# Kernel tuning notes

Hardware: AMD Instinct MI355X
Metric: run time of the kernel (lower is better)

Reference implementation:

```python
import jax, jax.numpy as jnp
import numpy as np

B, S, H = 4, 2048, 2048
NH, NKV, HD = 16, 4, 128  # heads, kv heads, head_dim; group g = NH // NKV = 4
ROPE_BASE = 10000.0


def rotate_half(x):
    x1, x2 = jnp.split(x, 2, axis=-1)
    return jnp.concatenate([-x2, x1], axis=-1)


def setup_inputs() -> dict:
    key = jax.random.key(0)
    k1, k2, k3 = jax.random.split(key, 3)
    hidden_states = jax.random.normal(k1, (B, S, H), dtype=jnp.float32)
    # additive causal mask [B, 1, S, S]: 0 on/below diagonal, large negative above
    causal = jnp.tril(jnp.ones((S, S), dtype=bool))
    attention_mask = jnp.where(causal, 0.0, -1e9).astype(jnp.float32)
    attention_mask = jnp.broadcast_to(attention_mask[None, None], (B, 1, S, S))
    # RoPE tables [S, HD]
    inv_freq = 1.0 / (ROPE_BASE ** (np.arange(0, HD, 2, dtype=np.float32) / HD))
    pos = np.arange(S, dtype=np.float32)
    freqs = np.outer(pos, inv_freq)                       # [S, HD/2]
    emb = np.concatenate([freqs, freqs], axis=-1)         # [S, HD]
    rope_cos = jnp.asarray(np.cos(emb), dtype=jnp.float32)
    rope_sin = jnp.asarray(np.sin(emb), dtype=jnp.float32)
    w_attn = jax.random.normal(k2, (H, H + 2 * NKV * HD), dtype=jnp.float32) * 0.02
    w_proj = jax.random.normal(k3, (H, H), dtype=jnp.float32) * 0.02
    return {"hidden_states": hidden_states, "attention_mask": attention_mask,
            "rope_cos": rope_cos, "rope_sin": rope_sin,
            "w_attn": w_attn, "w_proj": w_proj}


def reference(hidden_states, attention_mask, rope_cos, rope_sin, w_attn, w_proj):
    g = NH // NKV
    qkv = jnp.einsum('bsh,hf->bsf', hidden_states, w_attn)          # [B,S,(g+2)*NKV*HD]
    qkv = qkv.reshape(B, S, NKV, (g + 2) * HD)
    q, k, v = jnp.split(qkv, [g * HD, (g + 1) * HD], axis=-1)
    q = q.reshape(B, S, NH, HD).transpose(0, 2, 1, 3)               # [B,NH,S,HD]
    k = k.transpose(0, 2, 1, 3)                                     # [B,NKV,S,HD]
    v = v.transpose(0, 2, 1, 3)                                     # [B,NKV,S,HD]
    cos = rope_cos[None, None]                                      # [1,1,S,HD]
    sin = rope_sin[None, None]
    q = q * cos + rotate_half(q) * sin
    k = k * cos + rotate_half(k) * sin
    # repeat kv heads to match query heads (repeat_interleave semantics)
    k = jnp.repeat(k, g, axis=1)                                    # [B,NH,S,HD]
    v = jnp.repeat(v, g, axis=1)
    scale = 1.0 / (HD ** 0.5)
    scores = jnp.einsum('bhqd,bhkd->bhqk', q, k) * scale + attention_mask
    attn = jax.nn.softmax(scores.astype(jnp.float32), axis=-1).astype(q.dtype)
    out = jnp.einsum('bhqk,bhkd->bhqd', attn, v)                    # [B,NH,S,HD]
    out = out.transpose(0, 2, 1, 3).reshape(B, S, NH * HD)
    return jnp.einsum('bsh,hf->bsf', out, w_proj)
```

## Files before the change

kernel.cpp:

```cpp
#include <hip/hip_runtime.h>
#include <hip/hip_bf16.h>
#include <stdint.h>

#define B_   4
#define S_   2048
#define H_   2048
#define NH_  16
#define NKV_ 4
#define HD_  128
#define F_   3072

typedef __bf16 bf16x8 __attribute__((ext_vector_type(8)));
typedef float  f32x4  __attribute__((ext_vector_type(4)));
typedef unsigned short u16;

#define GLOAD_LDS16(gp, lp)                                                             \
  __builtin_amdgcn_global_load_lds((const __attribute__((address_space(1))) void*)(gp), \
                                   (__attribute__((address_space(3))) void*)(lp), 16, 0, 0)

__device__ __forceinline__ u16 f2bf(float f) {
  union { float f; uint32_t u; } v; v.f = f;
  uint32_t r = (v.u + 0x7FFFu + ((v.u >> 16) & 1u)) >> 16;
  return (u16)r;
}
__device__ __forceinline__ float bf2f(u16 u) {
  union { uint32_t u; float f; } v; v.u = ((uint32_t)u) << 16;
  return v.f;
}

__global__ void k_cvt_bf16(const float* __restrict__ in, u16* __restrict__ out, int n4) {
  int i = blockIdx.x * 256 + threadIdx.x;
  if (i >= n4) return;
  float4 v = ((const float4*)in)[i];
  union { u16 s[4]; uint2 u; } o;
  o.s[0] = f2bf(v.x); o.s[1] = f2bf(v.y); o.s[2] = f2bf(v.z); o.s[3] = f2bf(v.w);
  ((uint2*)out)[i] = o.u;
}

__global__ void k_transpose_cvt(const float* __restrict__ in, u16* __restrict__ out, int R, int C) {
  __shared__ u16 tile[64][68];
  int c0 = blockIdx.x * 64, r0 = blockIdx.y * 64;
  int t = threadIdx.x;
#pragma unroll
  for (int j = 0; j < 16; ++j) {
    int e = j * 256 + t;
    int r = e >> 6, c = e & 63;
    tile[r][c] = f2bf(in[(size_t)(r0 + r) * C + (c0 + c)]);
  }
  __syncthreads();
#pragma unroll
  for (int j = 0; j < 16; ++j) {
    int e = j * 256 + t;
    int c = e >> 6, r = e & 63;
    out[(size_t)(c0 + c) * R + (r0 + r)] = tile[r][c];
  }
}

template <bool OUTF32>
__global__ __launch_bounds__(256) void k_gemm_bt(const u16* __restrict__ A, const u16* __restrict__ BT,
                                                 void* __restrict__ Cv, int M, int N, int K) {
  __shared__ u16 lA[128 * 64];
  __shared__ u16 lB[128 * 64];
  int t = threadIdx.x, w = t >> 6, l = t & 63, c = l & 15, g = l >> 4;
  int bn = blockIdx.x * 128, bm = blockIdx.y * 128;
  int wm = (w >> 1) * 64, wn = (w & 1) * 64;

  f32x4 acc[4][4];
#pragma unroll
  for (int mi = 0; mi < 4; ++mi)
#pragma unroll
    for (int ni = 0; ni < 4; ++ni) acc[mi][ni] = (f32x4){0.f, 0.f, 0.f, 0.f};

  int nk = K >> 6;
  int srow = l >> 3, scol = (l & 7) * 8;
  for (int kt = 0; kt < nk; ++kt) {
    int k0 = kt << 6;
    __syncthreads();
#pragma unroll
    for (int i = 0; i < 4; ++i) {
      int ch = i * 4 + w;
      int row = ch * 8 + srow;
      GLOAD_LDS16(&A [(size_t)(bm + row) * K + k0 + scol], &lA[ch * 512]);
      GLOAD_LDS16(&BT[(size_t)(bn + row) * K + k0 + scol], &lB[ch * 512]);
    }
    asm volatile("s_waitcnt vmcnt(0)" ::: "memory");
    __syncthreads();
#pragma unroll
    for (int s = 0; s < 2; ++s) {
      bf16x8 af[4], bfr[4];
#pragma unroll
      for (int mi = 0; mi < 4; ++mi)
        af[mi] = *(const bf16x8*)&lA[(wm + mi * 16 + c) * 64 + (s * 4 + g) * 8];
#pragma unroll
      for (int ni = 0; ni < 4; ++ni)
        bfr[ni] = *(const bf16x8*)&lB[(wn + ni * 16 + c) * 64 + (s * 4 + g) * 8];
#pragma unroll
      for (int mi = 0; mi < 4; ++mi)
#pragma unroll
        for (int ni = 0; ni < 4; ++ni)
          acc[mi][ni] = __builtin_amdgcn_mfma_f32_16x16x32_bf16(af[mi], bfr[ni], acc[mi][ni], 0, 0, 0);
    }
  }
#pragma unroll
  for (int mi = 0; mi < 4; ++mi)
#pragma unroll
    for (int ni = 0; ni < 4; ++ni)
#pragma unroll
      for (int r = 0; r < 4; ++r) {
        size_t row = (size_t)bm + wm + mi * 16 + 4 * g + r;
        size_t col = (size_t)bn + wn + ni * 16 + c;
        if constexpr (OUTF32) ((float*)Cv)[row * N + col] = acc[mi][ni][r];
        else                  ((u16*)Cv)  [row * N + col] = f2bf(acc[mi][ni][r]);
      }
}

__global__ void k_rope_qk(const u16* __restrict__ qkv, const float* __restrict__ ct,
                          const float* __restrict__ st, u16* __restrict__ Q, u16* __restrict__ Kd) {
  size_t idx = (size_t)blockIdx.x * 256 + threadIdx.x;
  const size_t NQ = (size_t)B_ * NH_ * S_ * HD_;
  int d, s, row, col; size_t oidx; u16* dst;
  if (idx < NQ) {
    d = (int)(idx & 127); s = (int)((idx >> 7) & (S_ - 1));
    int h = (int)((idx >> 18) & 15); int b = (int)(idx >> 22);
    row = b * S_ + s;
    col = (h >> 2) * 768 + (h & 3) * 128 + d;
    dst = Q; oidx = idx;
  } else {
    size_t i2 = idx - NQ;
    d = (int)(i2 & 127); s = (int)((i2 >> 7) & (S_ - 1));
    int kvh = (int)((i2 >> 18) & 3); int b = (int)(i2 >> 20);
    row = b * S_ + s;
    col = kvh * 768 + 512 + d;
    dst = Kd; oidx = i2;
  }
  float x  = bf2f(qkv[(size_t)row * F_ + col]);
  float xr = (d < 64) ? -bf2f(qkv[(size_t)row * F_ + col + 64])
                      :  bf2f(qkv[(size_t)row * F_ + col - 64]);
  float o = x * ct[s * HD_ + d] + xr * st[s * HD_ + d];
  dst[oidx] = f2bf(o);
}

__global__ void k_transpose_v(const u16* __restrict__ qkv, u16* __restrict__ Vt) {
  __shared__ u16 tile[64][136];
  int s0 = blockIdx.x * 64;
  int b = blockIdx.y >> 2, kvh = blockIdx.y & 3;
  int t = threadIdx.x;
  const u16* src = qkv + (size_t)(b * S_ + s0) * F_ + kvh * 768 + 640;
#pragma unroll
  for (int j = 0; j < 4; ++j) {
    int e = j * 256 + t;
    int sl = e >> 4, ch = e & 15;
    *(uint4*)&tile[sl][ch * 8] = *(const uint4*)&src[(size_t)sl * F_ + ch * 8];
  }
  __syncthreads();
  u16* dstb = Vt + (size_t)(b * NKV_ + kvh) * HD_ * S_;
#pragma unroll
  for (int j = 0; j < 4; ++j) {
    int e = j * 256 + t;
    int d = e & 127, sc = e >> 7;
    u16 tmp[8];
#pragma unroll
    for (int i = 0; i < 8; ++i) tmp[i] = tile[sc * 8 + i][d];
    *(uint4*)&dstb[(size_t)d * S_ + s0 + sc * 8] = *(const uint4*)tmp;
  }
}

__global__ __launch_bounds__(256, 4) void k_flash(const u16* __restrict__ Q, const u16* __restrict__ K,
                                                  const u16* __restrict__ Vt, u16* __restrict__ O) {
  __shared__ u16 lK[64 * 128];
  __shared__ u16 lV[128 * 64];
  __shared__ u16 lP[4][16 * 64];
  int t = threadIdx.x, w = t >> 6, l = t & 63, c = l & 15, g = l >> 4;
  int qb = (int)(gridDim.x - 1 - blockIdx.x);
  int bh = blockIdx.y;
  int b = bh >> 4, h = bh & 15, kvh = h >> 2;
  int qw = qb * 64 + w * 16;
  const u16* Qb = Q  + (size_t)(b * NH_  + h)   * S_ * HD_;
  const u16* Kb = K  + (size_t)(b * NKV_ + kvh) * S_ * HD_;
  const u16* Vb = Vt + (size_t)(b * NKV_ + kvh) * HD_ * S_;

  bf16x8 qf[4];
#pragma unroll
  for (int sl = 0; sl < 4; ++sl)
    qf[sl] = *(const bf16x8*)&Qb[(size_t)(qw + c) * HD_ + sl * 32 + g * 8];

  f32x4 oacc[8];
#pragma unroll
  for (int nd = 0; nd < 8; ++nd) oacc[nd] = (f32x4){0.f, 0.f, 0.f, 0.f};
  float m_run = -1e30f, l_run = 0.f;

  int ntiles = qb + 1;
  int krl = l >> 4;
  int vrl = l >> 3;

  for (int kt = 0; kt < ntiles; ++kt) {
    int kv0 = kt * 64;
    __syncthreads();
#pragma unroll
    for (int i = 0; i < 4; ++i) {
      int ch = i * 4 + w;
      int rrK = ch * 4 + krl;
      int jK  = (l & 15) ^ (rrK & 15);
      GLOAD_LDS16(&Kb[(size_t)(kv0 + rrK) * HD_ + jK * 8], &lK[ch * 512]);
      int rdV = ch * 8 + vrl;
      int jV  = (l & 7) ^ (rdV & 7);
      GLOAD_LDS16(&Vb[(size_t)rdV * S_ + kv0 + jV * 8], &lV[ch * 512]);
    }
    asm volatile("s_waitcnt vmcnt(0)" ::: "memory");
    __syncthreads();
    if (kv0 <= qw + 15) {
      f32x4 sc[4];
#pragma unroll
      for (int f = 0; f < 4; ++f) sc[f] = (f32x4){0.f, 0.f, 0.f, 0.f};
#pragma unroll
      for (int sl = 0; sl < 4; ++sl)
#pragma unroll
        for (int f = 0; f < 4; ++f) {
          bf16x8 kf = *(const bf16x8*)&lK[(f * 16 + c) * 128 + (((sl * 4 + g) ^ c) * 8)];
          sc[f] = __builtin_amdgcn_mfma_f32_16x16x32_bf16(kf, qf[sl], sc[f], 0, 0, 0);
        }
      const float SCL = 0.088388347648318447f * 1.4426950408889634f;
      bool partial = (kv0 + 63 > qw);
      float pvv[4][4];
      float pm = -1e30f;
#pragma unroll
      for (int f = 0; f < 4; ++f)
#pragma unroll
        for (int r = 0; r < 4; ++r) {
          float v = sc[f][r] * SCL;
          if (partial && (kv0 + f * 16 + 4 * g + r > qw + c)) v = -1e30f;
          pvv[f][r] = v;
          pm = fmaxf(pm, v);
        }
      pm = fmaxf(pm, __shfl_xor(pm, 16));
      pm = fmaxf(pm, __shfl_xor(pm, 32));
      float m_new = fmaxf(m_run, pm);
      float alpha = exp2f(m_run - m_new);
      float ps = 0.f;
#pragma unroll
      for (int f = 0; f < 4; ++f)
#pragma unroll
        for (int r = 0; r < 4; ++r) {
          float p = exp2f(pvv[f][r] - m_new);
          pvv[f][r] = p;
          ps += p;
        }
      ps += __shfl_xor(ps, 16);
      ps += __shfl_xor(ps, 32);
      l_run = l_run * alpha + ps;
      m_run = m_new;
#pragma unroll
      for (int r = 0; r < 4; ++r) {
        float ar = __shfl(alpha, 4 * g + r);
#pragma unroll
        for (int nd = 0; nd < 8; ++nd) oacc[nd][r] *= ar;
      }
      char* Pw = (char*)&lP[w][0];
#pragma unroll
      for (int f = 0; f < 4; ++f) {
        int base = f * 32 + g * 8;
        int chunk = base >> 4, within = base & 15;
        uint32_t p01 = (uint32_t)f2bf(pvv[f][0]) | ((uint32_t)f2bf(pvv[f][1]) << 16);
        uint32_t p23 = (uint32_t)f2bf(pvv[f][2]) | ((uint32_t)f2bf(pvv[f][3]) << 16);
        int rowb = c * 128 + ((chunk ^ (c & 7)) << 4) + within;
        *(uint32_t*)(Pw + rowb)     = p01;
        *(uint32_t*)(Pw + rowb + 4) = p23;
      }
#pragma unroll
      for (int ks = 0; ks < 2; ++ks) {
        bf16x8 pf = *(const bf16x8*)(Pw + c * 128 + (((ks * 4 + g) ^ (c & 7)) << 4));
#pragma unroll
        for (int nd = 0; nd < 8; ++nd) {
          int rowv = nd * 16 + c;
          bf16x8 vf = *(const bf16x8*)&lV[rowv * 64 + (((ks * 4 + g) ^ (c & 7)) * 8)];
          oacc[nd] = __builtin_amdgcn_mfma_f32_16x16x32_bf16(pf, vf, oacc[nd], 0, 0, 0);
        }
      }
    }
  }
  float lr[4];
#pragma unroll
  for (int r = 0; r < 4; ++r) {
    float lv = __shfl(l_run, 4 * g + r);
    lr[r] = 1.f / lv;
  }
#pragma unroll
  for (int nd = 0; nd < 8; ++nd)
#pragma unroll
    for (int r = 0; r < 4; ++r) {
      size_t row = (size_t)b * S_ + (qw + 4 * g + r);
      O[row * (NH_ * HD_) + h * HD_ + nd * 16 + c] = f2bf(oacc[nd][r] * lr[r]);
    }
}

extern "C" void kernel_launch(void* const* d_in, const int* in_sizes, int n_in,
                              void* d_out, int out_size, void* d_ws, size_t ws_size,
                              hipStream_t stream) {
  const float* hid   = (const float*)d_in[0];
  const float* rcos  = (const float*)d_in[2];
  const float* rsin  = (const float*)d_in[3];
  const float* wattn = (const float*)d_in[4];
  const float* wproj = (const float*)d_in[5];

  u16* ws   = (u16*)d_ws;
  u16* hidB = ws;
  u16* wAT  = ws + 16777216;
  u16* wPT  = ws + 23068672;
  u16* qkv  = ws + 27262976;
  u16* Qs   = ws + 52428800;
  u16* Ks   = ws + 69206016;
  u16* Vts  = ws + 73400320;
  u16* Os   = qkv;

  k_cvt_bf16<<<16384, 256, 0, stream>>>(hid, hidB, 16777216 / 4);
  k_transpose_cvt<<<dim3(48, 32), 256, 0, stream>>>(wattn, wAT, 2048, 3072);
  k_transpose_cvt<<<dim3(32, 32), 256, 0, stream>>>(wproj, wPT, 2048, 2048);
  k_gemm_bt<false><<<dim3(24, 64), 256, 0, stream>>>(hidB, wAT, qkv, 8192, 3072, 2048);
  k_rope_qk<<<81920, 256, 0, stream>>>(qkv, rcos, rsin, Qs, Ks);
  k_transpose_v<<<dim3(32, 16), 256, 0, stream>>>(qkv, Vts);
  k_flash<<<dim3(32, 64), 256, 0, stream>>>(Qs, Ks, Vts, Os);
  k_gemm_bt<true><<<dim3(16, 64), 256, 0, stream>>>(Os, wPT, d_out, 8192, 2048, 2048);
}
```

Measured before the change: 680.8 us.

## Double-buffer LDS tiles in GEMM and flash attention, swizzle GEMM LDS

Both the bf16 GEMM and the flash-attention kernel now use two LDS buffers. The next K/V or A/B tile is issued with global_load_lds while MFMA work runs on the current tile, with one wait and barrier per iteration instead of two. The GEMM LDS layout also gets an XOR swizzle on 16-byte chunks to reduce bank conflicts on fragment reads. The doubled LDS footprint in the flash kernel leads to lowering its launch_bounds occupancy hint from 4 to 2 blocks per CU, which trades wave-level latency hiding for explicit prefetch.

Result: no change. 673.9 us (-1.0%).

```diff
diff --git a/kernel.cpp b/kernel.cpp
--- a/kernel.cpp
+++ b/kernel.cpp
@@ -59,8 +59,8 @@
 template <bool OUTF32>
 __global__ __launch_bounds__(256) void k_gemm_bt(const u16* __restrict__ A, const u16* __restrict__ BT,
                                                  void* __restrict__ Cv, int M, int N, int K) {
-  __shared__ u16 lA[128 * 64];
-  __shared__ u16 lB[128 * 64];
+  __shared__ u16 lA[2][128 * 64];
+  __shared__ u16 lB[2][128 * 64];
   int t = threadIdx.x, w = t >> 6, l = t & 63, c = l & 15, g = l >> 4;
   int bn = blockIdx.x * 128, bm = blockIdx.y * 128;
   int wm = (w >> 1) * 64, wn = (w & 1) * 64;
@@ -72,33 +72,48 @@
     for (int ni = 0; ni < 4; ++ni) acc[mi][ni] = (f32x4){0.f, 0.f, 0.f, 0.f};
 
   int nk = K >> 6;
-  int srow = l >> 3, scol = (l & 7) * 8;
+  int srow = l >> 3;
+  int scol = ((l & 7) ^ srow) * 8;
+
+#define GEMM_STAGE(k0, buf)                                                     \
+  _Pragma("unroll")                                                             \
+  for (int i = 0; i < 4; ++i) {                                                 \
+    int ch = i * 4 + w; int row = ch * 8 + srow;                                \
+    GLOAD_LDS16(&A [(size_t)(bm + row) * K + (k0) + scol], &lA[buf][ch * 512]); \
+    GLOAD_LDS16(&BT[(size_t)(bn + row) * K + (k0) + scol], &lB[buf][ch * 512]); \
+  }
+
+  GEMM_STAGE(0, 0)
+  asm volatile("s_waitcnt vmcnt(0)" ::: "memory");
+  __syncthreads();
+  int cur = 0;
   for (int kt = 0; kt < nk; ++kt) {
-    int k0 = kt << 6;
-    __syncthreads();
-#pragma unroll
-    for (int i = 0; i < 4; ++i) {
-      int ch = i * 4 + w;
-      int row = ch * 8 + srow;
-      GLOAD_LDS16(&A [(size_t)(bm + row) * K + k0 + scol], &lA[ch * 512]);
-      GLOAD_LDS16(&BT[(size_t)(bn + row) * K + k0 + scol], &lB[ch * 512]);
-    }
-    asm volatile("s_waitcnt vmcnt(0)" ::: "memory");
-    __syncthreads();
+    if (kt + 1 < nk) { GEMM_STAGE((kt + 1) << 6, cur ^ 1) }
+    const u16* cA = lA[cur];
+    const u16* cB = lB[cur];
 #pragma unroll
     for (int s = 0; s < 2; ++s) {
       bf16x8 af[4], bfr[4];
 #pragma unroll
-      for (int mi = 0; mi < 4; ++mi)
-        af[mi] = *(const bf16x8*)&lA[(wm + mi * 16 + c) * 64 + (s * 4 + g) * 8];
-#pragma unroll
-      for (int ni = 0; ni < 4; ++ni)
-        bfr[ni] = *(const bf16x8*)&lB[(wn + ni * 16 + c) * 64 + (s * 4 + g) * 8];
+      for (int mi = 0; mi < 4; ++mi) {
+        int row = wm + mi * 16 + c;
+        af[mi] = *(const bf16x8*)&cA[row * 64 + (((s * 4 + g) ^ (c & 7)) * 8)];
+      }
+#pragma unroll
+      for (int ni = 0; ni < 4; ++ni) {
+        int row = wn + ni * 16 + c;
+        bfr[ni] = *(const bf16x8*)&cB[row * 64 + (((s * 4 + g) ^ (c & 7)) * 8)];
+      }
 #pragma unroll
       for (int mi = 0; mi < 4; ++mi)
 #pragma unroll
         for (int ni = 0; ni < 4; ++ni)
           acc[mi][ni] = __builtin_amdgcn_mfma_f32_16x16x32_bf16(af[mi], bfr[ni], acc[mi][ni], 0, 0, 0);
+    }
+    if (kt + 1 < nk) {
+      asm volatile("s_waitcnt vmcnt(0)" ::: "memory");
+      __syncthreads();
+      cur ^= 1;
     }
   }
 #pragma unroll
@@ -112,6 +127,7 @@
         if constexpr (OUTF32) ((float*)Cv)[row * N + col] = acc[mi][ni][r];
         else                  ((u16*)Cv)  [row * N + col] = f2bf(acc[mi][ni][r]);
       }
+#undef GEMM_STAGE
 }
 
 __global__ void k_rope_qk(const u16* __restrict__ qkv, const float* __restrict__ ct,
@@ -165,10 +181,10 @@
   }
 }
 
-__global__ __launch_bounds__(256, 4) void k_flash(const u16* __restrict__ Q, const u16* __restrict__ K,
+__global__ __launch_bounds__(256, 2) void k_flash(const u16* __restrict__ Q, const u16* __restrict__ K,
                                                   const u16* __restrict__ Vt, u16* __restrict__ O) {
-  __shared__ u16 lK[64 * 128];
-  __shared__ u16 lV[128 * 64];
+  __shared__ u16 lK[2][64 * 128];
+  __shared__ u16 lV[2][128 * 64];
   __shared__ u16 lP[4][16 * 64];
   int t = threadIdx.x, w = t >> 6, l = t & 63, c = l & 15, g = l >> 4;
   int qb = (int)(gridDim.x - 1 - blockIdx.x);
@@ -193,22 +209,29 @@
   int krl = l >> 4;
   int vrl = l >> 3;
 
+#define STAGE_KV(kv0, buf)                                                           \
+  _Pragma("unroll")                                                                  \
+  for (int i = 0; i < 4; ++i) {                                                      \
+    int ch = i * 4 + w;                                                              \
+    int rrK = ch * 4 + krl;                                                          \
+    int jK  = (l & 15) ^ (rrK & 15);                                                 \
+    GLOAD_LDS16(&Kb[(size_t)((kv0) + rrK) * HD_ + jK * 8], &lK[buf][ch * 512]);      \
+    int rdV = ch * 8 + vrl;                                                          \
+    int jV  = (l & 7) ^ (rdV & 7);                                                   \
+    GLOAD_LDS16(&Vb[(size_t)rdV * S_ + (kv0) + jV * 8], &lV[buf][ch * 512]);         \
+  }
+
+  STAGE_KV(0, 0)
+  asm volatile("s_waitcnt vmcnt(0)" ::: "memory");
+  __syncthreads();
+  int cur = 0;
+
   for (int kt = 0; kt < ntiles; ++kt) {
     int kv0 = kt * 64;
-    __syncthreads();
-#pragma unroll
-    for (int i = 0; i < 4; ++i) {
-      int ch = i * 4 + w;
-      int rrK = ch * 4 + krl;
-      int jK  = (l & 15) ^ (rrK & 15);
-      GLOAD_LDS16(&Kb[(size_t)(kv0 + rrK) * HD_ + jK * 8], &lK[ch * 512]);
-      int rdV = ch * 8 + vrl;
-      int jV  = (l & 7) ^ (rdV & 7);
-      GLOAD_LDS16(&Vb[(size_t)rdV * S_ + kv0 + jV * 8], &lV[ch * 512]);
-    }
-    asm volatile("s_waitcnt vmcnt(0)" ::: "memory");
-    __syncthreads();
-    if (kv0 <= qw + 15) {
+    if (kt + 1 < ntiles) { STAGE_KV(kv0 + 64, cur ^ 1) }
+    {
+      const u16* cK = lK[cur];
+      const u16* cV = lV[cur];
       f32x4 sc[4];
 #pragma unroll
       for (int f = 0; f < 4; ++f) sc[f] = (f32x4){0.f, 0.f, 0.f, 0.f};
@@ -216,7 +239,7 @@
       for (int sl = 0; sl < 4; ++sl)
 #pragma unroll
         for (int f = 0; f < 4; ++f) {
-          bf16x8 kf = *(const bf16x8*)&lK[(f * 16 + c) * 128 + (((sl * 4 + g) ^ c) * 8)];
+          bf16x8 kf = *(const bf16x8*)&cK[(f * 16 + c) * 128 + (((sl * 4 + g) ^ c) * 8)];
           sc[f] = __builtin_amdgcn_mfma_f32_16x16x32_bf16(kf, qf[sl], sc[f], 0, 0, 0);
         }
       const float SCL = 0.088388347648318447f * 1.4426950408889634f;
@@ -272,12 +295,18 @@
 #pragma unroll
         for (int nd = 0; nd < 8; ++nd) {
           int rowv = nd * 16 + c;
-          bf16x8 vf = *(const bf16x8*)&lV[rowv * 64 + (((ks * 4 + g) ^ (c & 7)) * 8)];
+          bf16x8 vf = *(const bf16x8*)&cV[rowv * 64 + (((ks * 4 + g) ^ (c & 7)) * 8)];
           oacc[nd] = __builtin_amdgcn_mfma_f32_16x16x32_bf16(pf, vf, oacc[nd], 0, 0, 0);
         }
       }
     }
-  }
+    if (kt + 1 < ntiles) {
+      asm volatile("s_waitcnt vmcnt(0)" ::: "memory");
+      __syncthreads();
+      cur ^= 1;
+    }
+  }
+#undef STAGE_KV
   float lr[4];
 #pragma unroll
   for (int r = 0; r < 4; ++r) {
```
